# Optimization experiments

Hardware: AMD Instinct MI355X
Metric: run time of the kernel (lower is better)

## Reference

```python
import jax, jax.numpy as jnp
import numpy as np

N = 100000
E = 1600000
IN_C, HID_C, OUT_C = 128, 256, 64
EPS = 1e-5


def _glorot(key, shape):
    fan_in, fan_out = shape
    lim = float(np.sqrt(6.0 / (fan_in + fan_out)))
    return jax.random.uniform(key, shape, jnp.float32, -lim, lim)


def sage_conv(x, src, dst, deg_inv, W_l, b_l, W_r):
    # mean aggregation of neighbor features into target nodes
    msg_sum = jax.ops.segment_sum(x[src], dst, num_segments=N)  # [N, d]
    mean = msg_sum * deg_inv[:, None]
    return mean @ W_l + b_l + x @ W_r


def batch_norm(x, gamma, beta, rm, rv):
    return (x - rm) * jax.lax.rsqrt(rv + EPS) * gamma + beta


def setup_inputs() -> dict:
    key = jax.random.key(0)
    ks = jax.random.split(key, 10)
    x = jax.random.normal(ks[0], (N, IN_C), jnp.float32)
    edge_index = jax.random.randint(ks[1], (2, E), 0, N, jnp.int64)
    inp = {
        "x": x,
        "edge_index": edge_index,
        # layer 1: SAGEConv(IN_C -> HID_C) + BN
        "W1l": _glorot(ks[2], (IN_C, HID_C)),
        "b1l": jnp.zeros((HID_C,), jnp.float32),
        "W1r": _glorot(ks[3], (IN_C, HID_C)),
        "g1": jnp.ones((HID_C,), jnp.float32),
        "be1": jnp.zeros((HID_C,), jnp.float32),
        "rm1": 0.1 * jax.random.normal(ks[4], (HID_C,), jnp.float32),
        "rv1": jnp.ones((HID_C,), jnp.float32),
        # layer 2: SAGEConv(HID_C -> HID_C) + BN
        "W2l": _glorot(ks[5], (HID_C, HID_C)),
        "b2l": jnp.zeros((HID_C,), jnp.float32),
        "W2r": _glorot(ks[6], (HID_C, HID_C)),
        "g2": jnp.ones((HID_C,), jnp.float32),
        "be2": jnp.zeros((HID_C,), jnp.float32),
        "rm2": 0.1 * jax.random.normal(ks[7], (HID_C,), jnp.float32),
        "rv2": jnp.ones((HID_C,), jnp.float32),
        # classifier: SAGEConv(HID_C -> OUT_C)
        "Wcl": _glorot(ks[8], (HID_C, OUT_C)),
        "bcl": jnp.zeros((OUT_C,), jnp.float32),
        "Wcr": _glorot(ks[9], (HID_C, OUT_C)),
    }
    return inp


def reference(x, edge_index, W1l, b1l, W1r, g1, be1, rm1, rv1,
              W2l, b2l, W2r, g2, be2, rm2, rv2, Wcl, bcl, Wcr):
    src, dst = edge_index[0], edge_index[1]
    deg = jax.ops.segment_sum(jnp.ones((E,), jnp.float32), dst, num_segments=N)
    deg_inv = jnp.where(deg > 0, 1.0 / jnp.maximum(deg, 1.0), 0.0)

    h = sage_conv(x, src, dst, deg_inv, W1l, b1l, W1r)
    h = jax.nn.relu(batch_norm(h, g1, be1, rm1, rv1))
    # dropout is identity in eval mode (training=False)
    h = sage_conv(h, src, dst, deg_inv, W2l, b2l, W2r)
    h = jax.nn.relu(batch_norm(h, g2, be2, rm2, rv2))
    return sage_conv(h, src, dst, deg_inv, Wcl, bcl, Wcr)
```

## Files before the change

### kernel.cpp

```cpp
#include <hip/hip_runtime.h>
#include <stdint.h>

#define NN 100000
#define EE 1600000
#define IN_C 128
#define HID_C 256
#define OUT_C 64

#define NB 391
#define CAP 5120
#define K3_NPT 25
#define K3_BLOCKS 250

typedef unsigned short bf16_t;
typedef unsigned int u32;
typedef __attribute__((ext_vector_type(8))) short bf16x8;
typedef __attribute__((ext_vector_type(4))) float f32x4;

__device__ __forceinline__ float b2f(unsigned short u){
  unsigned int x = ((unsigned int)u) << 16;
  return __uint_as_float(x);
}
__device__ __forceinline__ unsigned short f2b(float f){
  unsigned int x = __float_as_uint(f);
  unsigned int r = x + 0x7FFFu + ((x >> 16) & 1u);
  return (unsigned short)(r >> 16);
}

#define GL16(gp, lp) __builtin_amdgcn_global_load_lds( \
    (const __attribute__((address_space(1))) void*)(gp), \
    (__attribute__((address_space(3))) void*)(lp), 16, 0, 0)

__global__ void detect_edge_k(const int* __restrict__ ei, int* __restrict__ eflag){
  __shared__ int sm[256];
  int t = threadIdx.x;
  int o = 0;
  for (int i = t; i < 1024; i += 256) o |= ei[2*i + 1];
  sm[t] = o; __syncthreads();
  for (int s = 128; s > 0; s >>= 1){
    if (t < s) sm[t] |= sm[t + s];
    __syncthreads();
  }
  if (t == 0) *eflag = (sm[0] == 0) ? 1 : 0;
}

__global__ __launch_bounds__(256) void bcount_k(const int* __restrict__ ei,
    const int* __restrict__ eflag, int* __restrict__ bcnt){
  __shared__ int h[NB];
  int t = threadIdx.x;
  for (int i = t; i < NB; i += 256) h[i] = 0;
  __syncthreads();
  int i64 = *eflag;
  int base = blockIdx.x * (256 * K3_NPT);
  #pragma unroll
  for (int q = 0; q < K3_NPT; ++q){
    int e = base + q * 256 + t;
    int d = i64 ? ei[2*(EE + e)] : ei[EE + e];
    atomicAdd(&h[d >> 8], 1);
  }
  __syncthreads();
  for (int i = t; i < NB; i += 256) if (h[i]) atomicAdd(&bcnt[i], h[i]);
}

__global__ void bscan_k(const int* __restrict__ bcnt, int* __restrict__ bbase){
  __shared__ int sm[512];
  int t = threadIdx.x;
  sm[t] = (t < NB) ? bcnt[t] : 0;
  __syncthreads();
  for (int off = 1; off < 512; off <<= 1){
    int a = (t >= off) ? sm[t - off] : 0;
    __syncthreads();
    sm[t] += a;
    __syncthreads();
  }
  if (t <= NB) bbase[t] = (t == 0) ? 0 : sm[t - 1];
}

__global__ __launch_bounds__(256) void bscatter_k(const int* __restrict__ ei,
    const int* __restrict__ eflag, const int* __restrict__ bbase,
    int* __restrict__ bfill, uint2* __restrict__ pairs){
  __shared__ int cnt[NB];
  __shared__ int cnt2[NB];
  __shared__ int lbase[NB];
  int t = threadIdx.x;
  for (int i = t; i < NB; i += 256){ cnt[i] = 0; cnt2[i] = 0; }
  __syncthreads();
  int i64 = *eflag;
  int ebase = blockIdx.x * (256 * K3_NPT);
  int src[K3_NPT], dst[K3_NPT];
  #pragma unroll
  for (int q = 0; q < K3_NPT; ++q){
    int e = ebase + q * 256 + t;
    src[q] = i64 ? ei[2*e] : ei[e];
    dst[q] = i64 ? ei[2*(EE + e)] : ei[EE + e];
    atomicAdd(&cnt[dst[q] >> 8], 1);
  }
  __syncthreads();
  for (int i = t; i < NB; i += 256)
    lbase[i] = cnt[i] ? atomicAdd(&bfill[i], cnt[i]) : 0;
  __syncthreads();
  #pragma unroll
  for (int q = 0; q < K3_NPT; ++q){
    int b = dst[q] >> 8;
    int r = atomicAdd(&cnt2[b], 1);
    pairs[bbase[b] + lbase[b] + r] = make_uint2((u32)src[q], (u32)dst[q]);
  }
}

__global__ __launch_bounds__(256) void bsort_k(const uint2* __restrict__ pairs,
    const int* __restrict__ bbase, int* __restrict__ rowptr, int* __restrict__ csr){
  __shared__ int hist[256];
  __shared__ int pref[257];
  __shared__ int cnt[256];
  __shared__ int lsrc[CAP];
  int b = blockIdx.x;
  int t = threadIdx.x;
  int e0 = bbase[b], e1 = bbase[b + 1];
  int s = e1 - e0;
  hist[t] = 0; cnt[t] = 0;
  __syncthreads();
  for (int i = t; i < s; i += 256)
    atomicAdd(&hist[pairs[e0 + i].y & 255], 1);
  __syncthreads();
  for (int off = 1; off < 256; off <<= 1){
    int a = (t >= off) ? hist[t - off] : 0;
    __syncthreads();
    hist[t] += a;
    __syncthreads();
  }
  if (t == 0) pref[0] = 0;
  pref[t + 1] = hist[t];
  __syncthreads();
  int gid = b * 256 + t;
  if (gid <= NN) rowptr[gid] = e0 + pref[t];
  for (int i = t; i < s; i += 256){
    uint2 p = pairs[e0 + i];
    int bin = p.y & 255;
    int r = atomicAdd(&cnt[bin], 1);
    int pos = pref[bin] + r;
    if (pos < CAP) lsrc[pos] = (int)p.x;
    else           csr[e0 + pos] = (int)p.x;
  }
  __syncthreads();
  int lim = s < CAP ? s : CAP;
  for (int i = t; i < lim; i += 256) csr[e0 + i] = lsrc[i];
}


__global__ void f2b_vec_k(const float* __restrict__ in, bf16_t* __restrict__ out, int n){
  int g = blockIdx.x * 256 + threadIdx.x;
  int i = g * 4;
  if (i < n){
    float4 v = *(const float4*)(in + i);
    uint2 u;
    u.x = (u32)f2b(v.x) | ((u32)f2b(v.y) << 16);
    u.y = (u32)f2b(v.z) | ((u32)f2b(v.w) << 16);
    *(uint2*)(out + i) = u;
  }
}

struct WtArgs {
  const float* W[6];
  bf16_t* Wt[6];
  int K[6], N[6];
  int off[7];
};

__global__ void wt_all_k(WtArgs a){
  int g = blockIdx.x * 256 + threadIdx.x;
  if (g >= a.off[6]) return;
  #pragma unroll
  for (int s = 0; s < 6; ++s){
    if (g >= a.off[s] && g < a.off[s + 1]){
      int local = g - a.off[s];
      int K = a.K[s], N = a.N[s];
      int n = local / K, k = local - n * K;
      a.Wt[s][local] = f2b(a.W[s][(size_t)k * N + n]);
    }
  }
}


template<int C, bool SIGNED, typename TIN>
__global__ __launch_bounds__(256) void quant_k(const TIN* __restrict__ in,
    uint8_t* __restrict__ outq, float* __restrict__ scales){
  constexpr int V = C / 64;
  int row  = (blockIdx.x * 256 + threadIdx.x) >> 6;
  int lane = threadIdx.x & 63;
  if (row >= NN) return;
  float v[V];
  if constexpr (sizeof(TIN) == 4){
    float2 u = *(const float2*)((const float*)in + (size_t)row * C + lane * 2);
    v[0] = u.x; v[1] = u.y;
  } else {
    const bf16_t* bp = (const bf16_t*)in + (size_t)row * C + lane * V;
    if constexpr (V == 4){
      uint2 u = *(const uint2*)bp;
      v[0] = b2f((unsigned short)(u.x & 0xffffu)); v[1] = b2f((unsigned short)(u.x >> 16));
      v[2] = b2f((unsigned short)(u.y & 0xffffu)); v[3] = b2f((unsigned short)(u.y >> 16));
    } else if constexpr (V == 2){
      u32 u = *(const u32*)bp;
      v[0] = b2f((unsigned short)(u & 0xffffu)); v[1] = b2f((unsigned short)(u >> 16));
    } else {
      v[0] = b2f(*bp);
    }
  }
  float m = 0.f;
  #pragma unroll
  for (int i = 0; i < V; ++i) m = fmaxf(m, SIGNED ? fabsf(v[i]) : v[i]);
  #pragma unroll
  for (int msk = 1; msk < 64; msk <<= 1) m = fmaxf(m, __shfl_xor(m, msk, 64));
  const float qmax = SIGNED ? 127.f : 255.f;
  float inv = m > 0.f ? qmax / m : 0.f;
  uint8_t qb[V];
  #pragma unroll
  for (int i = 0; i < V; ++i){
    float qf = rintf(v[i] * inv);
    if (SIGNED){
      qf = fminf(fmaxf(qf, -127.f), 127.f);
      qb[i] = (uint8_t)(int8_t)(int)qf;
    } else {
      qf = fminf(fmaxf(qf, 0.f), 255.f);
      qb[i] = (uint8_t)(int)qf;
    }
  }
  uint8_t* op = outq + (size_t)row * C + lane * V;
  if constexpr (V == 4){
    u32 p = (u32)qb[0] | ((u32)qb[1] << 8) | ((u32)qb[2] << 16) | ((u32)qb[3] << 24);
    *(u32*)op = p;
  } else if constexpr (V == 2){
    *(unsigned short*)op = (unsigned short)((u32)qb[0] | ((u32)qb[1] << 8));
  } else {
    *op = qb[0];
  }
  if (lane == 0) scales[row] = m / qmax;
}


__device__ __forceinline__ float qdec(u32 w, int b, bool sgn){
  u32 byte = (w >> (8 * b)) & 0xffu;
  return sgn ? (float)(int8_t)byte : (float)byte;
}

template<int C, bool SIGNED>
__global__ __launch_bounds__(256) void agg_q8_k(const uint8_t* __restrict__ tq,
    const float* __restrict__ tsc,
    const int* __restrict__ rowptr, const int* __restrict__ csr,
    bf16_t* __restrict__ outm){
  constexpr int V = C / 64;
  constexpr int B = 16;
  int wid  = (blockIdx.x * 256 + threadIdx.x) >> 6;
  int lane = threadIdx.x & 63;
  if (wid >= NN) return;
  int beg = __builtin_amdgcn_readfirstlane(rowptr[wid]);
  int end = __builtin_amdgcn_readfirstlane(rowptr[wid + 1]);
  float acc[V];
  #pragma unroll
  for (int i = 0; i < V; ++i) acc[i] = 0.f;

  const uint8_t* hb = tq + lane * V;
  int last = end - 1;
  for (int e = beg; e < end; e += B){
    int s[B]; float sc[B]; u32 w[B];
    #pragma unroll
    for (int q = 0; q < B; ++q){
      int idx = e + q;
      idx = idx < last ? idx : last;
      s[q] = csr[idx];
    }
    #pragma unroll
    for (int q = 0; q < B; ++q){
      if constexpr (V == 4) w[q] = *(const u32*)(hb + (size_t)s[q] * C);
      else                  w[q] = *(const unsigned short*)(hb + (size_t)s[q] * C);
      sc[q] = (e + q < end) ? tsc[s[q]] : 0.f;
    }
    #pragma unroll
    for (int q = 0; q < B; ++q)
      #pragma unroll
      for (int i = 0; i < V; ++i)
        acc[i] += sc[q] * qdec(w[q], i, SIGNED);
  }

  int d = end - beg;
  float di = d > 0 ? 1.0f / (float)d : 0.f;
  bf16_t* po = outm + (size_t)wid * C + lane * V;
  if constexpr (V == 2){
    u32 u = (u32)f2b(acc[0] * di) | ((u32)f2b(acc[1] * di) << 16);
    *(u32*)po = u;
  } else {
    uint2 u;
    u.x = (u32)f2b(acc[0] * di) | ((u32)f2b(acc[1] * di) << 16);
    u.y = (u32)f2b(acc[2] * di) | ((u32)f2b(acc[3] * di) << 16);
    *(uint2*)po = u;
  }
}


__global__ __launch_bounds__(256) void agg_final_q8_k(
    const uint8_t* __restrict__ Pq, const float* __restrict__ scp,
    const float* __restrict__ Q,
    const int* __restrict__ rowptr, const int* __restrict__ csr,
    float* __restrict__ out){
  constexpr int B = 16;
  int wid  = (blockIdx.x * 256 + threadIdx.x) >> 6;
  int lane = threadIdx.x & 63;
  if (wid >= NN) return;
  int beg = __builtin_amdgcn_readfirstlane(rowptr[wid]);
  int end = __builtin_amdgcn_readfirstlane(rowptr[wid + 1]);
  const uint8_t* Pb = Pq + lane;
  float acc = 0.f;
  int last = end - 1;
  for (int e = beg; e < end; e += B){
    int s[B]; uint8_t b[B]; float sc[B];
    #pragma unroll
    for (int q = 0; q < B; ++q){
      int idx = e + q;
      idx = idx < last ? idx : last;
      s[q] = csr[idx];
    }
    #pragma unroll
    for (int q = 0; q < B; ++q){
      b[q] = Pb[(size_t)s[q] * 64];
      sc[q] = (e + q < end) ? scp[s[q]] : 0.f;
    }
    #pragma unroll
    for (int q = 0; q < B; ++q) acc += sc[q] * (float)(int8_t)b[q];
  }
  int d = end - beg;
  float di = d > 0 ? 1.0f / (float)d : 0.f;
  out[(size_t)wid * 64 + lane] = acc * di + Q[(size_t)wid * 64 + lane];
}


template<int K_>
__global__ __launch_bounds__(256) void mfma_gemm_k(
    const bf16_t* __restrict__ A0, const bf16_t* __restrict__ A1,
    const bf16_t* __restrict__ W0t, const bf16_t* __restrict__ W1t,
    const float* __restrict__ bias,
    const float* __restrict__ gamma, const float* __restrict__ beta,
    const float* __restrict__ rmean, const float* __restrict__ rvar,
    bf16_t* __restrict__ out, int M, int Nout)
{
  constexpr int BM = 128;
  constexpr int BN = 128;
  constexpr int BK = 64;
  constexpr int KT = K_ / BK;
  constexpr int T  = 2 * KT;
  __shared__ bf16_t As[2][BM * BK];
  __shared__ bf16_t Bs[2][BN * BK];

  int t    = threadIdx.x;
  int lane = t & 63;
  int wid  = t >> 6;
  int wr   = wid >> 1, wc = wid & 1;
  int l15  = lane & 15;
  int quad = lane >> 4;

  int m0 = blockIdx.x * BM;
  int n0 = blockIdx.y * BN;

  f32x4 acc[4][4];
  #pragma unroll
  for (int i = 0; i < 4; ++i)
    #pragma unroll
    for (int j = 0; j < 4; ++j)
      acc[i][j] = (f32x4){0.f, 0.f, 0.f, 0.f};

  auto stage = [&](int tile, int buf){
    const bf16_t* Ap = (tile < KT) ? A0 : A1;
    const bf16_t* Wp = (tile < KT) ? W0t : W1t;
    int k0 = ((tile < KT) ? tile : tile - KT) * BK;
    #pragma unroll
    for (int i = 0; i < 4; ++i){
      int c   = i * 256 + t;
      int row = c >> 3;
      int k8  = (c & 7) ^ (row & 7);
      int gm  = m0 + row; gm = gm < NN ? gm : NN - 1;
      GL16(Ap + (size_t)gm * K_ + k0 + k8 * 8, &As[buf][(i * 256 + (t & 192)) * 8]);
    }
    #pragma unroll
    for (int i = 0; i < 4; ++i){
      int c   = i * 256 + t;
      int row = c >> 3;
      int k8  = (c & 7) ^ (row & 7);
      GL16(Wp + (size_t)(n0 + row) * K_ + k0 + k8 * 8, &Bs[buf][(i * 256 + (t & 192)) * 8]);
    }
  };

  stage(0, 0);
  #pragma unroll
  for (int tile = 0; tile < T; ++tile){
    int buf = tile & 1;
    if (tile + 1 < T){
      stage(tile + 1, buf ^ 1);
      asm volatile("s_waitcnt vmcnt(8)" ::: "memory");
    } else {
      asm volatile("s_waitcnt vmcnt(0)" ::: "memory");
    }
    __builtin_amdgcn_s_barrier();
    #pragma unroll
    for (int kk = 0; kk < 2; ++kk){
      bf16x8 af[4], bfr[4];
      #pragma unroll
      for (int i = 0; i < 4; ++i){
        int row = wr * 64 + i * 16 + l15;
        af[i] = *(const bf16x8*)(&As[buf][(size_t)((row << 3) + ((quad + kk * 4) ^ (row & 7))) * 8]);
      }
      #pragma unroll
      for (int j = 0; j < 4; ++j){
        int row = wc * 64 + j * 16 + l15;
        bfr[j] = *(const bf16x8*)(&Bs[buf][(size_t)((row << 3) + ((quad + kk * 4) ^ (row & 7))) * 8]);
      }
      #pragma unroll
      for (int i = 0; i < 4; ++i)
        #pragma unroll
        for (int j = 0; j < 4; ++j)
          acc[i][j] = __builtin_amdgcn_mfma_f32_16x16x32_bf16(af[i], bfr[j], acc[i][j], 0, 0, 0);
    }
    __builtin_amdgcn_s_barrier();
  }

  #pragma unroll
  for (int j = 0; j < 4; ++j){
    int col = n0 + wc * 64 + j * 16 + l15;
    float sc = gamma[col] * rsqrtf(rvar[col] + 1e-5f);
    float shift = (bias[col] - rmean[col]) * sc + beta[col];
    #pragma unroll
    for (int i = 0; i < 4; ++i){
      int rbase = m0 + wr * 64 + i * 16 + quad * 4;
      #pragma unroll
      for (int r = 0; r < 4; ++r){
        int row = rbase + r;
        if (row < M){
          float v = fmaxf(acc[i][j][r] * sc + shift, 0.f);
          out[(size_t)row * Nout + col] = f2b(v);
        }
      }
    }
  }
}


__global__ __launch_bounds__(256) void gemm3_k(
    const bf16_t* __restrict__ A, const bf16_t* __restrict__ Wt,
    const float* __restrict__ bcl,
    bf16_t* __restrict__ P, float* __restrict__ Q, int M)
{
  constexpr int K_ = 256, BM = 128, BN = 128, BK = 64;
  constexpr int T = K_ / BK;
  __shared__ bf16_t As[2][BM * BK];
  __shared__ bf16_t Bs[2][BN * BK];

  int t    = threadIdx.x;
  int lane = t & 63;
  int wid  = t >> 6;
  int wr   = wid >> 1, wc = wid & 1;
  int l15  = lane & 15;
  int quad = lane >> 4;
  int m0 = blockIdx.x * BM;

  f32x4 acc[4][4];
  #pragma unroll
  for (int i = 0; i < 4; ++i)
    #pragma unroll
    for (int j = 0; j < 4; ++j)
      acc[i][j] = (f32x4){0.f, 0.f, 0.f, 0.f};

  auto stage = [&](int tile, int buf){
    int k0 = tile * BK;
    #pragma unroll
    for (int i = 0; i < 4; ++i){
      int c   = i * 256 + t;
      int row = c >> 3;
      int k8  = (c & 7) ^ (row & 7);
      int gm  = m0 + row; gm = gm < NN ? gm : NN - 1;
      GL16(A + (size_t)gm * K_ + k0 + k8 * 8, &As[buf][(i * 256 + (t & 192)) * 8]);
    }
    #pragma unroll
    for (int i = 0; i < 4; ++i){
      int c   = i * 256 + t;
      int row = c >> 3;
      int k8  = (c & 7) ^ (row & 7);
      GL16(Wt + (size_t)row * K_ + k0 + k8 * 8, &Bs[buf][(i * 256 + (t & 192)) * 8]);
    }
  };

  stage(0, 0);
  #pragma unroll
  for (int tile = 0; tile < T; ++tile){
    int buf = tile & 1;
    if (tile + 1 < T){
      stage(tile + 1, buf ^ 1);
      asm volatile("s_waitcnt vmcnt(8)" ::: "memory");
    } else {
      asm volatile("s_waitcnt vmcnt(0)" ::: "memory");
    }
    __builtin_amdgcn_s_barrier();
    #pragma unroll
    for (int kk = 0; kk < 2; ++kk){
      bf16x8 af[4], bfr[4];
      #pragma unroll
      for (int i = 0; i < 4; ++i){
        int row = wr * 64 + i * 16 + l15;
        af[i] = *(const bf16x8*)(&As[buf][(size_t)((row << 3) + ((quad + kk * 4) ^ (row & 7))) * 8]);
      }
      #pragma unroll
      for (int j = 0; j < 4; ++j){
        int row = wc * 64 + j * 16 + l15;
        bfr[j] = *(const bf16x8*)(&Bs[buf][(size_t)((row << 3) + ((quad + kk * 4) ^ (row & 7))) * 8]);
      }
      #pragma unroll
      for (int i = 0; i < 4; ++i)
        #pragma unroll
        for (int j = 0; j < 4; ++j)
          acc[i][j] = __builtin_amdgcn_mfma_f32_16x16x32_bf16(af[i], bfr[j], acc[i][j], 0, 0, 0);
    }
    __builtin_amdgcn_s_barrier();
  }

  #pragma unroll
  for (int j = 0; j < 4; ++j){
    int col = wc * 64 + j * 16 + l15;
    #pragma unroll
    for (int i = 0; i < 4; ++i){
      int rbase = m0 + wr * 64 + i * 16 + quad * 4;
      #pragma unroll
      for (int r = 0; r < 4; ++r){
        int row = rbase + r;
        if (row < M){
          float v = acc[i][j][r];
          if (col < 64) P[(size_t)row * 64 + col] = f2b(v);
          else          Q[(size_t)row * 64 + (col - 64)] = v + bcl[col - 64];
        }
      }
    }
  }
}


extern "C" void kernel_launch(void* const* d_in, const int* in_sizes, int n_in,
                              void* d_out, int out_size, void* d_ws, size_t ws_size,
                              hipStream_t stream)
{
  const float* x   = (const float*)d_in[0];
  const int*   ei  = (const int*)d_in[1];
  const float* W1l = (const float*)d_in[2];
  const float* b1l = (const float*)d_in[3];
  const float* W1r = (const float*)d_in[4];
  const float* g1  = (const float*)d_in[5];
  const float* be1 = (const float*)d_in[6];
  const float* rm1 = (const float*)d_in[7];
  const float* rv1 = (const float*)d_in[8];
  const float* W2l = (const float*)d_in[9];
  const float* b2l = (const float*)d_in[10];
  const float* W2r = (const float*)d_in[11];
  const float* g2  = (const float*)d_in[12];
  const float* be2 = (const float*)d_in[13];
  const float* rm2 = (const float*)d_in[14];
  const float* rv2 = (const float*)d_in[15];
  const float* Wcl = (const float*)d_in[16];
  const float* bcl = (const float*)d_in[17];
  const float* Wcr = (const float*)d_in[18];
  (void)in_sizes; (void)n_in; (void)out_size; (void)ws_size;

  char* ws = (char*)d_ws;
  size_t off = 0;
  auto alloc = [&](size_t bytes)->char* {
    char* p = ws + off;
    off += (bytes + 15) & ~(size_t)15;
    return p;
  };
  int*    bcnt   = (int*)   alloc(800 * 4);
  int*    bfill  = bcnt + 400;
  int*    bbase  = (int*)   alloc((size_t)(NB + 1) * 4);
  int*    rowptr = (int*)   alloc((size_t)(NN + 1) * 4);
  int*    eflag  = (int*)   alloc(16);
  int*    csr    = (int*)   alloc((size_t)EE * 4);
  bf16_t* xb     = (bf16_t*)alloc((size_t)NN * IN_C * 2);
  bf16_t* aggb   = (bf16_t*)alloc((size_t)NN * HID_C * 2);
  bf16_t* h1     = (bf16_t*)alloc((size_t)NN * HID_C * 2);
  bf16_t* h2     = (bf16_t*)alloc((size_t)NN * HID_C * 2);
  bf16_t* W1lt   = (bf16_t*)alloc((size_t)IN_C  * HID_C * 2);
  bf16_t* W1rt   = (bf16_t*)alloc((size_t)IN_C  * HID_C * 2);
  bf16_t* W2lt   = (bf16_t*)alloc((size_t)HID_C * HID_C * 2);
  bf16_t* W2rt   = (bf16_t*)alloc((size_t)HID_C * HID_C * 2);
  bf16_t* Wc3t   = (bf16_t*)alloc((size_t)128 * HID_C * 2);
  float*  sc1    = (float*) alloc((size_t)NN * 4);
  float*  scp    = (float*) alloc((size_t)NN * 4);

  uint2*   pairs = (uint2*)aggb;
  uint8_t* xq  = (uint8_t*)h2;
  float*   scx = (float*)((char*)h2 + (size_t)NN * IN_C);
  uint8_t* h1q = (uint8_t*)xb;
  bf16_t*  P   = xb;
  uint8_t* Pq  = (uint8_t*)aggb;
  float*   Q   = (float*)h1;

  hipMemsetAsync(bcnt, 0, 800 * 4, stream);

  f2b_vec_k<<<(NN * IN_C / 4 + 255) / 256, 256, 0, stream>>>(x, xb, NN * IN_C);
  WtArgs wa;
  wa.W[0] = W1l; wa.Wt[0] = W1lt; wa.K[0] = IN_C;  wa.N[0] = HID_C;
  wa.W[1] = W1r; wa.Wt[1] = W1rt; wa.K[1] = IN_C;  wa.N[1] = HID_C;
  wa.W[2] = W2l; wa.Wt[2] = W2lt; wa.K[2] = HID_C; wa.N[2] = HID_C;
  wa.W[3] = W2r; wa.Wt[3] = W2rt; wa.K[3] = HID_C; wa.N[3] = HID_C;
  wa.W[4] = Wcl; wa.Wt[4] = Wc3t;             wa.K[4] = HID_C; wa.N[4] = OUT_C;
  wa.W[5] = Wcr; wa.Wt[5] = Wc3t + 64 * 256;  wa.K[5] = HID_C; wa.N[5] = OUT_C;
  wa.off[0] = 0;
  for (int s = 0; s < 6; ++s) wa.off[s + 1] = wa.off[s] + wa.K[s] * wa.N[s];
  wt_all_k<<<(wa.off[6] + 255) / 256, 256, 0, stream>>>(wa);

  detect_edge_k<<<1, 256, 0, stream>>>(ei, eflag);
  bcount_k<<<K3_BLOCKS, 256, 0, stream>>>(ei, eflag, bcnt);
  bscan_k<<<1, 512, 0, stream>>>(bcnt, bbase);
  bscatter_k<<<K3_BLOCKS, 256, 0, stream>>>(ei, eflag, bbase, bfill, pairs);
  bsort_k<<<NB, 256, 0, stream>>>(pairs, bbase, rowptr, csr);

  int wb = (NN + 3) / 4;
  int mblocks = (NN + 127) / 128;

  quant_k<IN_C, true, float><<<wb, 256, 0, stream>>>(x, xq, scx);
  agg_q8_k<IN_C, true><<<wb, 256, 0, stream>>>(xq, scx, rowptr, csr, aggb);
  dim3 g1d(mblocks, HID_C / 128);
  mfma_gemm_k<IN_C><<<g1d, 256, 0, stream>>>(
      aggb, xb, W1lt, W1rt, b1l, g1, be1, rm1, rv1, h1, NN, HID_C);

  quant_k<HID_C, false, bf16_t><<<wb, 256, 0, stream>>>(h1, h1q, sc1);
  agg_q8_k<HID_C, false><<<wb, 256, 0, stream>>>(h1q, sc1, rowptr, csr, aggb);
  mfma_gemm_k<HID_C><<<g1d, 256, 0, stream>>>(
      aggb, h1, W2lt, W2rt, b2l, g2, be2, rm2, rv2, h2, NN, HID_C);

  gemm3_k<<<mblocks, 256, 0, stream>>>(h2, Wc3t, bcl, P, Q, NN);
  quant_k<OUT_C, true, bf16_t><<<wb, 256, 0, stream>>>(P, Pq, scp);
  agg_final_q8_k<<<wb, 256, 0, stream>>>(Pq, scp, Q, rowptr, csr, (float*)d_out);
}
```

Measured before the change: 644.5 us.

## Split wavefront into edge groups with 16-byte row loads and shuffle reduction

The int8 aggregation kernels now split each wavefront into groups of lanes, each group covering one edge. Each lane loads a 16-byte chunk of the neighbor row instead of 1–4 bytes, and partial sums are combined with xor-shuffle reductions at the end. The goal is wider memory transactions and more edges in flight per wavefront for gather-bound aggregation. In exchange it adds a cross-lane reduction of 16 accumulators per node, leaves few lanes active on the final store, and wastes lanes on low-degree nodes when a group runs past the edge count.

```diff
diff --git a/kernel.cpp b/kernel.cpp
--- a/kernel.cpp
+++ b/kernel.cpp
@@ -237,61 +237,60 @@
 }
 
 
-__device__ __forceinline__ float qdec(u32 w, int b, bool sgn){
-  u32 byte = (w >> (8 * b)) & 0xffu;
-  return sgn ? (float)(int8_t)byte : (float)byte;
-}
-
 template<int C, bool SIGNED>
 __global__ __launch_bounds__(256) void agg_q8_k(const uint8_t* __restrict__ tq,
     const float* __restrict__ tsc,
     const int* __restrict__ rowptr, const int* __restrict__ csr,
     bf16_t* __restrict__ outm){
-  constexpr int V = C / 64;
-  constexpr int B = 16;
+  constexpr int L = C / 16;
+  constexpr int G = 64 / L;
   int wid  = (blockIdx.x * 256 + threadIdx.x) >> 6;
   int lane = threadIdx.x & 63;
   if (wid >= NN) return;
   int beg = __builtin_amdgcn_readfirstlane(rowptr[wid]);
   int end = __builtin_amdgcn_readfirstlane(rowptr[wid + 1]);
-  float acc[V];
-  #pragma unroll
-  for (int i = 0; i < V; ++i) acc[i] = 0.f;
-
-  const uint8_t* hb = tq + lane * V;
+  int g = lane / L;
+  int r = lane % L;
+
+  float acc[16];
+  #pragma unroll
+  for (int i = 0; i < 16; ++i) acc[i] = 0.f;
+
   int last = end - 1;
-  for (int e = beg; e < end; e += B){
-    int s[B]; float sc[B]; u32 w[B];
-    #pragma unroll
-    for (int q = 0; q < B; ++q){
-      int idx = e + q;
-      idx = idx < last ? idx : last;
-      s[q] = csr[idx];
-    }
-    #pragma unroll
-    for (int q = 0; q < B; ++q){
-      if constexpr (V == 4) w[q] = *(const u32*)(hb + (size_t)s[q] * C);
-      else                  w[q] = *(const unsigned short*)(hb + (size_t)s[q] * C);
-      sc[q] = (e + q < end) ? tsc[s[q]] : 0.f;
-    }
-    #pragma unroll
-    for (int q = 0; q < B; ++q)
-      #pragma unroll
-      for (int i = 0; i < V; ++i)
-        acc[i] += sc[q] * qdec(w[q], i, SIGNED);
-  }
+  for (int e = beg; e < end; e += G){
+    int idx = e + g;
+    int cl  = idx < last ? idx : last;
+    int s_  = csr[cl];
+    float sv = tsc[s_];
+    float sc = idx < end ? sv : 0.f;
+    uint4 w = *(const uint4*)(tq + (size_t)s_ * C + r * 16);
+    u32 ws[4] = {w.x, w.y, w.z, w.w};
+    #pragma unroll
+    for (int b = 0; b < 4; ++b)
+      #pragma unroll
+      for (int j = 0; j < 4; ++j){
+        u32 byte = (ws[b] >> (8 * j)) & 0xffu;
+        float v = SIGNED ? (float)(int)(int8_t)(uint8_t)byte : (float)byte;
+        acc[b * 4 + j] += sc * v;
+      }
+  }
+
+  #pragma unroll
+  for (int mask = L; mask < 64; mask <<= 1)
+    #pragma unroll
+    for (int i = 0; i < 16; ++i)
+      acc[i] += __shfl_xor(acc[i], mask, 64);
 
   int d = end - beg;
   float di = d > 0 ? 1.0f / (float)d : 0.f;
-  bf16_t* po = outm + (size_t)wid * C + lane * V;
-  if constexpr (V == 2){
-    u32 u = (u32)f2b(acc[0] * di) | ((u32)f2b(acc[1] * di) << 16);
-    *(u32*)po = u;
-  } else {
-    uint2 u;
-    u.x = (u32)f2b(acc[0] * di) | ((u32)f2b(acc[1] * di) << 16);
-    u.y = (u32)f2b(acc[2] * di) | ((u32)f2b(acc[3] * di) << 16);
-    *(uint2*)po = u;
+  if (lane < L){
+    bf16_t* po = outm + (size_t)wid * C + lane * 16;
+    u32 o[8];
+    #pragma unroll
+    for (int i = 0; i < 8; ++i)
+      o[i] = (u32)f2b(acc[2 * i] * di) | ((u32)f2b(acc[2 * i + 1] * di) << 16);
+    *(uint4*)(po)     = make_uint4(o[0], o[1], o[2], o[3]);
+    *(uint4*)(po + 8) = make_uint4(o[4], o[5], o[6], o[7]);
   }
 }
 
@@ -301,34 +300,52 @@
     const float* __restrict__ Q,
     const int* __restrict__ rowptr, const int* __restrict__ csr,
     float* __restrict__ out){
-  constexpr int B = 16;
+  constexpr int L = 4, G = 16;
   int wid  = (blockIdx.x * 256 + threadIdx.x) >> 6;
   int lane = threadIdx.x & 63;
   if (wid >= NN) return;
   int beg = __builtin_amdgcn_readfirstlane(rowptr[wid]);
   int end = __builtin_amdgcn_readfirstlane(rowptr[wid + 1]);
-  const uint8_t* Pb = Pq + lane;
-  float acc = 0.f;
+  int g = lane >> 2;
+  int r = lane & 3;
+
+  float acc[16];
+  #pragma unroll
+  for (int i = 0; i < 16; ++i) acc[i] = 0.f;
+
   int last = end - 1;
-  for (int e = beg; e < end; e += B){
-    int s[B]; uint8_t b[B]; float sc[B];
-    #pragma unroll
-    for (int q = 0; q < B; ++q){
-      int idx = e + q;
-      idx = idx < last ? idx : last;
-      s[q] = csr[idx];
-    }
-    #pragma unroll
-    for (int q = 0; q < B; ++q){
-      b[q] = Pb[(size_t)s[q] * 64];
-      sc[q] = (e + q < end) ? scp[s[q]] : 0.f;
-    }
-    #pragma unroll
-    for (int q = 0; q < B; ++q) acc += sc[q] * (float)(int8_t)b[q];
-  }
+  for (int e = beg; e < end; e += G){
+    int idx = e + g;
+    int cl  = idx < last ? idx : last;
+    int s_  = csr[cl];
+    float sv = scp[s_];
+    float sc = idx < end ? sv : 0.f;
+    uint4 w = *(const uint4*)(Pq + (size_t)s_ * 64 + r * 16);
+    u32 ws[4] = {w.x, w.y, w.z, w.w};
+    #pragma unroll
+    for (int b = 0; b < 4; ++b)
+      #pragma unroll
+      for (int j = 0; j < 4; ++j){
+        u32 byte = (ws[b] >> (8 * j)) & 0xffu;
+        acc[b * 4 + j] += sc * (float)(int)(int8_t)(uint8_t)byte;
+      }
+  }
+
+  #pragma unroll
+  for (int mask = L; mask < 64; mask <<= 1)
+    #pragma unroll
+    for (int i = 0; i < 16; ++i)
+      acc[i] += __shfl_xor(acc[i], mask, 64);
+
   int d = end - beg;
   float di = d > 0 ? 1.0f / (float)d : 0.f;
-  out[(size_t)wid * 64 + lane] = acc * di + Q[(size_t)wid * 64 + lane];
+  if (lane < L){
+    float* po = out + (size_t)wid * 64 + lane * 16;
+    const float* qo = Q + (size_t)wid * 64 + lane * 16;
+    #pragma unroll
+    for (int i = 0; i < 16; ++i)
+      po[i] = acc[i] * di + qo[i];
+  }
 }
 
 
```

Result: faster. 614.2 us (-4.7%).
